# Kernel optimization log

Hardware: AMD Instinct MI355X
Metric: run time of the kernel (lower is better)

## Reference

```python
import jax, jax.numpy as jnp
import numpy as np

N_HEADS = 16
D_MODEL = 1024
D_K = D_MODEL // N_HEADS
NEG_INF = -1e9


def setup_inputs() -> dict:
    key = jax.random.key(0)
    ks = jax.random.split(key, 7)
    B, S, D = 4, 2048, D_MODEL
    scale = 1.0 / np.sqrt(D)
    return {
        "query": jax.random.normal(ks[0], (B, S, D), dtype=jnp.float32),
        "key": jax.random.normal(ks[1], (B, S, D), dtype=jnp.float32),
        "value": jax.random.normal(ks[2], (B, S, D), dtype=jnp.float32),
        "Wq": jax.random.normal(ks[3], (D, D), dtype=jnp.float32) * scale,
        "Wk": jax.random.normal(ks[4], (D, D), dtype=jnp.float32) * scale,
        "Wv": jax.random.normal(ks[5], (D, D), dtype=jnp.float32) * scale,
        "Wo": jax.random.normal(ks[6], (D, D), dtype=jnp.float32) * scale,
    }


def _split_heads(x):
    # (B, S, D) -> (B, H, S, d_k)
    B, S, _ = x.shape
    return x.reshape(B, S, N_HEADS, D_K).transpose(0, 2, 1, 3)


def reference(query, key, value, Wq, Wk, Wv, Wo):
    B, S, D = query.shape
    # nn.Linear(d, d, bias=False): y = x @ W.T ; here W is stored as [out, in]
    Q = _split_heads(query @ Wq.T)
    K = _split_heads(key @ Wk.T)
    V = _split_heads(value @ Wv.T)
    scores = jnp.einsum("bhqd,bhkd->bhqk", Q, K) / jnp.sqrt(jnp.float32(D_K))
    # causal mask: 0 on/below diagonal, -1e9 above
    causal = jnp.where(
        jnp.tril(jnp.ones((S, S), dtype=bool)), 0.0, NEG_INF
    ).astype(scores.dtype)
    scores = scores + causal[None, None, :, :]
    attn = jax.nn.softmax(scores, axis=-1)
    heads = jnp.einsum("bhqk,bhkd->bhqd", attn, V)
    concat = heads.transpose(0, 2, 1, 3).reshape(B, S, D)
    out = concat @ Wo.T
    return out  # dropout p=0.0 -> identity
```

## Files before the change

kernel.cpp:

```cpp
#include <hip/hip_runtime.h>
#include <hip/hip_bf16.h>

typedef short short8 __attribute__((ext_vector_type(8)));
typedef short short4v __attribute__((ext_vector_type(4)));
typedef float floatx4 __attribute__((ext_vector_type(4)));

constexpr int BATCH = 4;
constexpr int SEQ = 2048;
constexpr int DMODEL = 1024;
constexpr int NHEADS = 16;
constexpr int DKH = 64;
constexpr int MROWS = BATCH * SEQ;
constexpr size_t NE = (size_t)MROWS * DMODEL;
constexpr size_t WE = (size_t)DMODEL * DMODEL;
constexpr float SC = 0.18033688011112042f;

__device__ __forceinline__ short f2bf(float f) {
    unsigned u = __float_as_uint(f);
    u += 0x7fffu + ((u >> 16) & 1u);
    return (short)(u >> 16);
}

__device__ __forceinline__ short2 pk2(float a, float b) {
    __hip_bfloat162 h = __float22bfloat162_rn(float2{a, b});
    short2 r;
    __builtin_memcpy(&r, &h, 4);
    return r;
}

__device__ __forceinline__ void ld16(const void* g, void* l) {
    __builtin_amdgcn_global_load_lds(
        (const __attribute__((address_space(1))) unsigned int*)g,
        (__attribute__((address_space(3))) unsigned int*)l, 16, 0, 0);
}

__global__ __launch_bounds__(256) void f32_to_bf16(const float* __restrict__ s,
                                                   short* __restrict__ d, int n4) {
    int i = blockIdx.x * blockDim.x + threadIdx.x;
    const int stride = gridDim.x * blockDim.x;
    for (; i < n4; i += stride) {
        float4 f = ((const float4*)s)[i];
        short4v v;
        v[0] = f2bf(f.x); v[1] = f2bf(f.y); v[2] = f2bf(f.z); v[3] = f2bf(f.w);
        ((short4v*)d)[i] = v;
    }
}

__global__ __launch_bounds__(256) void cvt2(const float* __restrict__ s0,
                                            const float* __restrict__ s1,
                                            short* __restrict__ d0,
                                            short* __restrict__ d1, int n4) {
    const float* s = blockIdx.y ? s1 : s0;
    short* d = blockIdx.y ? d1 : d0;
    int i = blockIdx.x * blockDim.x + threadIdx.x;
    const int stride = gridDim.x * blockDim.x;
    for (; i < n4; i += stride) {
        float4 f = ((const float4*)s)[i];
        short4v v;
        v[0] = f2bf(f.x); v[1] = f2bf(f.y); v[2] = f2bf(f.z); v[3] = f2bf(f.w);
        ((short4v*)d)[i] = v;
    }
}

__global__ __launch_bounds__(256) void wcvt3(const float* __restrict__ a,
                                             const float* __restrict__ b,
                                             const float* __restrict__ c,
                                             short* __restrict__ dst, int n4) {
    const float* s = (blockIdx.y == 0) ? a : (blockIdx.y == 1) ? b : c;
    const float m = (blockIdx.y == 0) ? SC : 1.0f;
    short* d = dst + (size_t)blockIdx.y * (size_t)n4 * 4;
    int i = blockIdx.x * blockDim.x + threadIdx.x;
    const int stride = gridDim.x * blockDim.x;
    for (; i < n4; i += stride) {
        float4 f = ((const float4*)s)[i];
        short4v v;
        v[0] = f2bf(f.x * m); v[1] = f2bf(f.y * m);
        v[2] = f2bf(f.z * m); v[3] = f2bf(f.w * m);
        ((short4v*)d)[i] = v;
    }
}

template <int OUT_MODE>
__device__ __forceinline__ void gemm_body(const short* __restrict__ A,
                                          const short* __restrict__ B,
                                          void* __restrict__ Yp) {
    __shared__ __align__(16) short Asw[2][128 * 32];
    __shared__ __align__(16) short Bsw[2][128 * 32];

    const int tid = threadIdx.x;
    const int w = tid >> 6, l = tid & 63;
    const int lane16 = l & 15, quad = l >> 4;
    const int wm = (w >> 1) * 64, wn = (w & 1) * 64;
    const int m0 = blockIdx.x * 128, n0 = blockIdx.y * 128;
    const int fsw = (lane16 >> 1) & 3;

    auto stage = [&](int k0, int bufi) {
#pragma unroll
        for (int i = 0; i < 2; ++i) {
            const int id = i * 256 + tid;
            const int row = id >> 2, ch = id & 3;
            const int sch = ch ^ ((row >> 1) & 3);
            ld16(A + (size_t)(m0 + row) * DMODEL + k0 + sch * 8,
                 &Asw[bufi][(i * 256 + w * 64) * 8]);
            ld16(B + (size_t)(n0 + row) * DMODEL + k0 + sch * 8,
                 &Bsw[bufi][(i * 256 + w * 64) * 8]);
        }
    };

    floatx4 acc[4][4];
#pragma unroll
    for (int i = 0; i < 4; ++i)
#pragma unroll
        for (int j = 0; j < 4; ++j) acc[i][j] = {0.f, 0.f, 0.f, 0.f};

    constexpr int NT = DMODEL / 32;
    stage(0, 0);
    __syncthreads();

    for (int t = 0; t < NT; ++t) {
        const int cur = t & 1;
        if (t + 1 < NT) stage((t + 1) * 32, cur ^ 1);

        short8 af[4], bfr[4];
#pragma unroll
        for (int mi = 0; mi < 4; ++mi)
            af[mi] = *(const short8*)(&Asw[cur][(wm + mi * 16 + lane16) * 32 +
                                                ((quad ^ fsw) * 8)]);
#pragma unroll
        for (int ni = 0; ni < 4; ++ni)
            bfr[ni] = *(const short8*)(&Bsw[cur][(wn + ni * 16 + lane16) * 32 +
                                                 ((quad ^ fsw) * 8)]);
#pragma unroll
        for (int mi = 0; mi < 4; ++mi)
#pragma unroll
            for (int ni = 0; ni < 4; ++ni)
                acc[mi][ni] = __builtin_amdgcn_mfma_f32_16x16x32_bf16(af[mi], bfr[ni],
                                                                      acc[mi][ni], 0, 0, 0);
        __syncthreads();
    }

    const int gmb = m0 + wm, gnb = n0 + wn;
    if (OUT_MODE == 0) {
        short* Y = (short*)Yp;
#pragma unroll
        for (int mi = 0; mi < 4; ++mi)
#pragma unroll
            for (int ni = 0; ni < 4; ++ni) {
                const int gm = gmb + mi * 16 + quad * 4;
                const int gn = gnb + ni * 16 + lane16;
#pragma unroll
                for (int r = 0; r < 4; ++r)
                    Y[(size_t)(gm + r) * DMODEL + gn] = f2bf(acc[mi][ni][r]);
            }
    } else if (OUT_MODE == 1) {
        short* Y = (short*)Yp;
#pragma unroll
        for (int mi = 0; mi < 4; ++mi)
#pragma unroll
            for (int ni = 0; ni < 4; ++ni) {
                const int gm = gmb + mi * 16 + quad * 4;
                const int gn = gnb + ni * 16 + lane16;
                const int bb = gm >> 11, ss = gm & (SEQ - 1);
                const int hh = gn >> 6, dd = gn & 63;
                const size_t base = ((size_t)(bb * NHEADS + hh) * DKH + dd) * SEQ + ss;
                short4v vv;
#pragma unroll
                for (int r = 0; r < 4; ++r) vv[r] = f2bf(acc[mi][ni][r]);
                *(short4v*)(Y + base) = vv;
            }
    } else {
        float* Y = (float*)Yp;
#pragma unroll
        for (int mi = 0; mi < 4; ++mi)
#pragma unroll
            for (int ni = 0; ni < 4; ++ni) {
                const int gm = gmb + mi * 16 + quad * 4;
                const int gn = gnb + ni * 16 + lane16;
#pragma unroll
                for (int r = 0; r < 4; ++r)
                    Y[(size_t)(gm + r) * DMODEL + gn] = acc[mi][ni][r];
            }
    }
}

template <int OUT_MODE>
__global__ __launch_bounds__(256, 3) void gemm_nt(const short* __restrict__ A,
                                                  const short* __restrict__ B,
                                                  void* __restrict__ Yp) {
    gemm_body<OUT_MODE>(A, B, Yp);
}

__global__ __launch_bounds__(256, 3) void gemm_qk(const short* __restrict__ Aq,
                                                  const short* __restrict__ Ak,
                                                  const short* __restrict__ Wqk,
                                                  short* __restrict__ Yq,
                                                  short* __restrict__ Yk) {
    const int z = blockIdx.z;
    gemm_body<0>(z ? Ak : Aq, Wqk + (size_t)z * WE, z ? Yk : Yq);
}

__global__ __launch_bounds__(256, 4) void attn_fwd(const short* __restrict__ Qb,
                                                   const short* __restrict__ Kb,
                                                   const short* __restrict__ Vt,
                                                   short* __restrict__ Oc) {
    __shared__ __align__(16) short Kl[2][64 * 64];
    __shared__ __align__(16) short Vl[2][64 * 64];
    __shared__ __align__(16) short Plds[4][16][64];

    const int bh = blockIdx.x;
    const int qt = (int)(gridDim.y - 1) - blockIdx.y;
    const int b = bh >> 4, h = bh & 15;
    const int tid = threadIdx.x;
    const int w = tid >> 6, l = tid & 63;
    const int lane16 = l & 15, quad = l >> 4;

    const short* Qrow =
        Qb + ((size_t)b * SEQ + qt * 64 + w * 16 + lane16) * DMODEL + h * DKH;
    const short8 qf0 = *(const short8*)(Qrow + quad * 8);
    const short8 qf1 = *(const short8*)(Qrow + 32 + quad * 8);

    const int r0 = tid >> 3, c0 = tid & 7;
    const int sc0 = c0 ^ (r0 & 7);
    const short* Kg = Kb + (size_t)b * SEQ * DMODEL + h * DKH;
    const short* Vg = Vt + (size_t)bh * DKH * SEQ;

    short8 kra, krb, vra, vrb;
    kra = *(const short8*)(Kg + (size_t)r0 * DMODEL + c0 * 8);
    krb = *(const short8*)(Kg + (size_t)(r0 + 32) * DMODEL + c0 * 8);
    vra = *(const short8*)(Vg + (size_t)r0 * SEQ + c0 * 8);
    vrb = *(const short8*)(Vg + (size_t)(r0 + 32) * SEQ + c0 * 8);
    *(short8*)&Kl[0][r0 * 64 + sc0 * 8] = kra;
    *(short8*)&Kl[0][(r0 + 32) * 64 + sc0 * 8] = krb;
    *(short8*)&Vl[0][r0 * 64 + sc0 * 8] = vra;
    *(short8*)&Vl[0][(r0 + 32) * 64 + sc0 * 8] = vrb;
    if (qt > 0) {
        kra = *(const short8*)(Kg + (size_t)(64 + r0) * DMODEL + c0 * 8);
        krb = *(const short8*)(Kg + (size_t)(64 + r0 + 32) * DMODEL + c0 * 8);
        vra = *(const short8*)(Vg + (size_t)r0 * SEQ + 64 + c0 * 8);
        vrb = *(const short8*)(Vg + (size_t)(r0 + 32) * SEQ + 64 + c0 * 8);
    }

    floatx4 oacc[4];
#pragma unroll
    for (int ni = 0; ni < 4; ++ni) oacc[ni] = {0.f, 0.f, 0.f, 0.f};
    float Lp = 0.f;
    const int swz = lane16 & 7;
    const int psw = lane16 & 7;

    for (int kt = 0; kt <= qt; ++kt) {
        const int cur = kt & 1;
        __syncthreads();
        if (kt < qt) {
            const int nb = cur ^ 1;
            *(short8*)&Kl[nb][r0 * 64 + sc0 * 8] = kra;
            *(short8*)&Kl[nb][(r0 + 32) * 64 + sc0 * 8] = krb;
            *(short8*)&Vl[nb][r0 * 64 + sc0 * 8] = vra;
            *(short8*)&Vl[nb][(r0 + 32) * 64 + sc0 * 8] = vrb;
            if (kt + 1 < qt) {
                const int kn = (kt + 2) * 64;
                kra = *(const short8*)(Kg + (size_t)(kn + r0) * DMODEL + c0 * 8);
                krb = *(const short8*)(Kg + (size_t)(kn + r0 + 32) * DMODEL + c0 * 8);
                vra = *(const short8*)(Vg + (size_t)r0 * SEQ + kn + c0 * 8);
                vrb = *(const short8*)(Vg + (size_t)(r0 + 32) * SEQ + kn + c0 * 8);
            }
        }

        float p[4][4];
#pragma unroll
        for (int nt = 0; nt < 4; ++nt) {
            const short* kr = &Kl[cur][(nt * 16 + lane16) * 64];
            floatx4 st = {0.f, 0.f, 0.f, 0.f};
            st = __builtin_amdgcn_mfma_f32_16x16x32_bf16(
                *(const short8*)(kr + (quad ^ swz) * 8), qf0, st, 0, 0, 0);
            st = __builtin_amdgcn_mfma_f32_16x16x32_bf16(
                *(const short8*)(kr + ((4 + quad) ^ swz) * 8), qf1, st, 0, 0, 0);
#pragma unroll
            for (int r = 0; r < 4; ++r) p[nt][r] = st[r];
        }

#pragma unroll
        for (int nt = 0; nt < 4; ++nt)
#pragma unroll
            for (int r = 0; r < 4; ++r) p[nt][r] = __builtin_amdgcn_exp2f(p[nt][r]);

        if (kt == qt) {
            const int qloc = w * 16 + lane16;
#pragma unroll
            for (int nt = 0; nt < 4; ++nt)
#pragma unroll
                for (int r = 0; r < 4; ++r)
                    if (nt * 16 + quad * 4 + r > qloc) p[nt][r] = 0.f;
        }

        float rs01 = 0.f, rs23 = 0.f;
#pragma unroll
        for (int nt = 0; nt < 4; ++nt)
#pragma unroll
            for (int r = 0; r < 4; ++r) {
                if (nt < 2) rs01 += p[nt][r]; else rs23 += p[nt][r];
            }
        Lp += rs01 + rs23;

#pragma unroll
        for (int nt = 0; nt < 4; ++nt) {
            const short2 lo = pk2(p[nt][0], p[nt][1]);
            const short2 hi = pk2(p[nt][2], p[nt][3]);
            short4v pk;
            pk[0] = lo.x; pk[1] = lo.y; pk[2] = hi.x; pk[3] = hi.y;
            const int pch = (nt * 2 + (quad >> 1)) ^ psw;
            *(short4v*)&Plds[w][lane16][pch * 8 + (quad & 1) * 4] = pk;
        }
        const short8 pf0 = *(const short8*)&Plds[w][lane16][(quad ^ psw) * 8];
        const short8 pf1 = *(const short8*)&Plds[w][lane16][((4 + quad) ^ psw) * 8];

#pragma unroll
        for (int ni = 0; ni < 4; ++ni) {
            const short* vr = &Vl[cur][(ni * 16 + lane16) * 64];
            oacc[ni] = __builtin_amdgcn_mfma_f32_16x16x32_bf16(
                pf0, *(const short8*)(vr + (quad ^ swz) * 8), oacc[ni], 0, 0, 0);
            oacc[ni] = __builtin_amdgcn_mfma_f32_16x16x32_bf16(
                pf1, *(const short8*)(vr + ((4 + quad) ^ swz) * 8), oacc[ni], 0, 0, 0);
        }
    }

    float L = Lp + __shfl_xor(Lp, 16);
    L += __shfl_xor(L, 32);
    float linv[4];
#pragma unroll
    for (int r = 0; r < 4; ++r) linv[r] = 1.f / __shfl(L, quad * 4 + r);
#pragma unroll
    for (int r = 0; r < 4; ++r) {
        const int qg = qt * 64 + w * 16 + quad * 4 + r;
#pragma unroll
        for (int ni = 0; ni < 4; ++ni)
            Oc[((size_t)b * SEQ + qg) * DMODEL + h * DKH + ni * 16 + lane16] =
                f2bf(oacc[ni][r] * linv[r]);
    }
}

extern "C" void kernel_launch(void* const* d_in, const int* in_sizes, int n_in,
                              void* d_out, int out_size, void* d_ws, size_t ws_size,
                              hipStream_t stream) {
    const float* q = (const float*)d_in[0];
    const float* k = (const float*)d_in[1];
    const float* v = (const float*)d_in[2];
    const float* Wq = (const float*)d_in[3];
    const float* Wk = (const float*)d_in[4];
    const float* Wv = (const float*)d_in[5];
    const float* Wo = (const float*)d_in[6];

    short* Qb = (short*)d_ws;
    short* Kb = Qb + NE;
    short* Vt = Kb + NE;
    short* Cc = Vt + NE;
    short* Wqb = (short*)d_out;
    short* Wkb = Wqb + WE;
    short* Wvb = Wqb + 2 * WE;
    short* Kbf = Wqb + 3 * WE;
    short* Wob = Vt;

    dim3 gg(MROWS / 128, DMODEL / 128);
    dim3 gqk(MROWS / 128, DMODEL / 128, 2);
    dim3 ga(BATCH * NHEADS, SEQ / 64);
    const int actN4 = (int)(NE / 4), wN4 = (int)(WE / 4);

    wcvt3<<<dim3(256, 3), 256, 0, stream>>>(Wq, Wk, Wv, (short*)d_out, wN4);
    cvt2<<<dim3(1024, 2), 256, 0, stream>>>(q, k, Cc, Kbf, actN4);
    gemm_qk<<<gqk, 256, 0, stream>>>(Cc, Kbf, Wqb, Qb, Kb);
    f32_to_bf16<<<2048, 256, 0, stream>>>(v, Cc, actN4);
    gemm_nt<1><<<gg, 256, 0, stream>>>(Cc, Wvb, Vt);
    attn_fwd<<<ga, 256, 0, stream>>>(Qb, Kb, Vt, Cc);
    f32_to_bf16<<<512, 256, 0, stream>>>(Wo, Wob, wN4);
    gemm_nt<2><<<gg, 256, 0, stream>>>(Cc, Wob, d_out);
}
```

Measured before the change: 312.0 us.

## Use 256x256 GEMM tiles with 8 waves and interleaved split-K LDS pipeline

Enlarges the projection GEMM block tile from 128x128 to 256x256 and uses 512 threads (8 waves, each computing 128x64). Each 64-wide K step is split into two 32-wide sub-stages whose global-to-LDS loads are interleaved with the MFMA phases. Hand-written vmcnt waits plus barriers replace __syncthreads, and s_setprio raises priority around the MFMA bursts. The aim is more operand reuse per LDS byte and better overlap of loads with compute. The trade-off is that the V and output GEMMs now launch only 128 blocks on a 256-CU device, and register and LDS pressure per block rise.

Measured after the change: 328.5 us. +5.3%, slower.

```diff
diff --git a/kernel.cpp b/kernel.cpp
--- a/kernel.cpp
+++ b/kernel.cpp
@@ -32,6 +32,19 @@
     __builtin_amdgcn_global_load_lds(
         (const __attribute__((address_space(1))) unsigned int*)g,
         (__attribute__((address_space(3))) unsigned int*)l, 16, 0, 0);
+}
+
+__device__ __forceinline__ void sync_vm4() {
+    asm volatile("s_waitcnt vmcnt(4)" ::: "memory");
+    __builtin_amdgcn_sched_barrier(0);
+    __builtin_amdgcn_s_barrier();
+    __builtin_amdgcn_sched_barrier(0);
+}
+__device__ __forceinline__ void sync_vm0() {
+    asm volatile("s_waitcnt vmcnt(0)" ::: "memory");
+    __builtin_amdgcn_sched_barrier(0);
+    __builtin_amdgcn_s_barrier();
+    __builtin_amdgcn_sched_barrier(0);
 }
 
 __global__ __launch_bounds__(256) void f32_to_bf16(const float* __restrict__ s,
@@ -80,70 +93,99 @@
     }
 }
 
+template <int MH, int KS, bool RB>
+__device__ __forceinline__ void do_phase(const short* Ab, const short* Bb,
+                                         floatx4 (&acc)[8][4], short8 (&bfr)[4],
+                                         int wmw, int wnw, int lane16, int quad,
+                                         int fsw) {
+    if (RB) {
+#pragma unroll
+        for (int ni = 0; ni < 4; ++ni) {
+            const int row = wnw + ni * 16 + lane16;
+            bfr[ni] = *(const short8*)&Bb[KS * (256 * 32) + row * 32 +
+                                          ((quad ^ fsw) * 8)];
+        }
+    }
+    short8 af[4];
+#pragma unroll
+    for (int i = 0; i < 4; ++i) {
+        const int row = wmw + MH * 64 + i * 16 + lane16;
+        af[i] = *(const short8*)&Ab[KS * (256 * 32) + row * 32 +
+                                    ((quad ^ fsw) * 8)];
+    }
+    __builtin_amdgcn_s_setprio(1);
+#pragma unroll
+    for (int i = 0; i < 4; ++i)
+#pragma unroll
+        for (int ni = 0; ni < 4; ++ni)
+            acc[MH * 4 + i][ni] = __builtin_amdgcn_mfma_f32_16x16x32_bf16(
+                af[i], bfr[ni], acc[MH * 4 + i][ni], 0, 0, 0);
+    __builtin_amdgcn_s_setprio(0);
+}
+
 template <int OUT_MODE>
-__device__ __forceinline__ void gemm_body(const short* __restrict__ A,
-                                          const short* __restrict__ B,
-                                          void* __restrict__ Yp) {
-    __shared__ __align__(16) short Asw[2][128 * 32];
-    __shared__ __align__(16) short Bsw[2][128 * 32];
+__device__ __forceinline__ void gemm_body(const short* A, const short* B,
+                                          void* Yp) {
+    __shared__ __align__(16) short Asw[2][2][256 * 32];
+    __shared__ __align__(16) short Bsw[2][2][256 * 32];
 
     const int tid = threadIdx.x;
     const int w = tid >> 6, l = tid & 63;
     const int lane16 = l & 15, quad = l >> 4;
-    const int wm = (w >> 1) * 64, wn = (w & 1) * 64;
-    const int m0 = blockIdx.x * 128, n0 = blockIdx.y * 128;
+    const int wmw = (w >> 2) * 128, wnw = (w & 3) * 64;
+    const int m0 = blockIdx.x * 256, n0 = blockIdx.y * 256;
     const int fsw = (lane16 >> 1) & 3;
 
-    auto stage = [&](int k0, int bufi) {
-#pragma unroll
-        for (int i = 0; i < 2; ++i) {
-            const int id = i * 256 + tid;
-            const int row = id >> 2, ch = id & 3;
-            const int sch = ch ^ ((row >> 1) & 3);
-            ld16(A + (size_t)(m0 + row) * DMODEL + k0 + sch * 8,
-                 &Asw[bufi][(i * 256 + w * 64) * 8]);
-            ld16(B + (size_t)(n0 + row) * DMODEL + k0 + sch * 8,
-                 &Bsw[bufi][(i * 256 + w * 64) * 8]);
-        }
+    const int rr = tid >> 2;
+    const int cc = (tid & 3) ^ ((rr >> 1) & 3);
+    const int ldsA0 = (w * 64) * 8, ldsA1 = (512 + w * 64) * 8;
+
+    auto stA = [&](int k0, int bufi, int ks) {
+        const short* g = A + (size_t)m0 * DMODEL + k0 + ks * 32 + cc * 8;
+        ld16(g + (size_t)rr * DMODEL, &Asw[bufi][ks][ldsA0]);
+        ld16(g + (size_t)(rr + 128) * DMODEL, &Asw[bufi][ks][ldsA1]);
     };
-
-    floatx4 acc[4][4];
-#pragma unroll
-    for (int i = 0; i < 4; ++i)
+    auto stB = [&](int k0, int bufi, int ks) {
+        const short* g = B + (size_t)n0 * DMODEL + k0 + ks * 32 + cc * 8;
+        ld16(g + (size_t)rr * DMODEL, &Bsw[bufi][ks][ldsA0]);
+        ld16(g + (size_t)(rr + 128) * DMODEL, &Bsw[bufi][ks][ldsA1]);
+    };
+
+    floatx4 acc[8][4];
+#pragma unroll
+    for (int i = 0; i < 8; ++i)
 #pragma unroll
         for (int j = 0; j < 4; ++j) acc[i][j] = {0.f, 0.f, 0.f, 0.f};
 
-    constexpr int NT = DMODEL / 32;
-    stage(0, 0);
-    __syncthreads();
-
+    constexpr int NT = DMODEL / 64;
+    stA(0, 0, 0); stB(0, 0, 0); stA(0, 0, 1); stB(0, 0, 1);
+    sync_vm4();
+
+    short8 bfr[4];
     for (int t = 0; t < NT; ++t) {
-        const int cur = t & 1;
-        if (t + 1 < NT) stage((t + 1) * 32, cur ^ 1);
-
-        short8 af[4], bfr[4];
-#pragma unroll
-        for (int mi = 0; mi < 4; ++mi)
-            af[mi] = *(const short8*)(&Asw[cur][(wm + mi * 16 + lane16) * 32 +
-                                                ((quad ^ fsw) * 8)]);
-#pragma unroll
-        for (int ni = 0; ni < 4; ++ni)
-            bfr[ni] = *(const short8*)(&Bsw[cur][(wn + ni * 16 + lane16) * 32 +
-                                                 ((quad ^ fsw) * 8)]);
-#pragma unroll
-        for (int mi = 0; mi < 4; ++mi)
-#pragma unroll
-            for (int ni = 0; ni < 4; ++ni)
-                acc[mi][ni] = __builtin_amdgcn_mfma_f32_16x16x32_bf16(af[mi], bfr[ni],
-                                                                      acc[mi][ni], 0, 0, 0);
-        __syncthreads();
-    }
-
-    const int gmb = m0 + wm, gnb = n0 + wn;
+        const int cur = t & 1, nxt = cur ^ 1;
+        const short* Ab = &Asw[cur][0][0];
+        const short* Bb = &Bsw[cur][0][0];
+        const int k1 = (t + 1) * 64;
+        const bool more = (t + 1 < NT);
+
+        if (more) stA(k1, nxt, 0);
+        do_phase<0, 0, true>(Ab, Bb, acc, bfr, wmw, wnw, lane16, quad, fsw);
+        if (more) stB(k1, nxt, 0);
+        do_phase<1, 0, false>(Ab, Bb, acc, bfr, wmw, wnw, lane16, quad, fsw);
+        if (more) sync_vm4(); else sync_vm0();
+        if (more) stA(k1, nxt, 1);
+        do_phase<0, 1, true>(Ab, Bb, acc, bfr, wmw, wnw, lane16, quad, fsw);
+        if (more) stB(k1, nxt, 1);
+        do_phase<1, 1, false>(Ab, Bb, acc, bfr, wmw, wnw, lane16, quad, fsw);
+        if (more) sync_vm4();
+    }
+
+    const int gmb = m0 + wmw, gnb = n0 + wnw;
     if (OUT_MODE == 0) {
         short* Y = (short*)Yp;
 #pragma unroll
-        for (int mi = 0; mi < 4; ++mi)
+        for (int mi = 0; mi < 8; ++mi)
 #pragma unroll
             for (int ni = 0; ni < 4; ++ni) {
                 const int gm = gmb + mi * 16 + quad * 4;
@@ -155,7 +197,7 @@
     } else if (OUT_MODE == 1) {
         short* Y = (short*)Yp;
 #pragma unroll
-        for (int mi = 0; mi < 4; ++mi)
+        for (int mi = 0; mi < 8; ++mi)
 #pragma unroll
             for (int ni = 0; ni < 4; ++ni) {
                 const int gm = gmb + mi * 16 + quad * 4;
@@ -171,7 +213,7 @@
     } else {
         float* Y = (float*)Yp;
 #pragma unroll
-        for (int mi = 0; mi < 4; ++mi)
+        for (int mi = 0; mi < 8; ++mi)
 #pragma unroll
             for (int ni = 0; ni < 4; ++ni) {
                 const int gm = gmb + mi * 16 + quad * 4;
@@ -184,13 +226,13 @@
 }
 
 template <int OUT_MODE>
-__global__ __launch_bounds__(256, 3) void gemm_nt(const short* __restrict__ A,
+__global__ __launch_bounds__(512, 2) void gemm_nt(const short* __restrict__ A,
                                                   const short* __restrict__ B,
                                                   void* __restrict__ Yp) {
     gemm_body<OUT_MODE>(A, B, Yp);
 }
 
-__global__ __launch_bounds__(256, 3) void gemm_qk(const short* __restrict__ Aq,
+__global__ __launch_bounds__(512, 2) void gemm_qk(const short* __restrict__ Aq,
                                                   const short* __restrict__ Ak,
                                                   const short* __restrict__ Wqk,
                                                   short* __restrict__ Yq,
@@ -359,17 +401,17 @@
     short* Kbf = Wqb + 3 * WE;
     short* Wob = Vt;
 
-    dim3 gg(MROWS / 128, DMODEL / 128);
-    dim3 gqk(MROWS / 128, DMODEL / 128, 2);
+    dim3 gg(MROWS / 256, DMODEL / 256);
+    dim3 gqk(MROWS / 256, DMODEL / 256, 2);
     dim3 ga(BATCH * NHEADS, SEQ / 64);
     const int actN4 = (int)(NE / 4), wN4 = (int)(WE / 4);
 
     wcvt3<<<dim3(256, 3), 256, 0, stream>>>(Wq, Wk, Wv, (short*)d_out, wN4);
     cvt2<<<dim3(1024, 2), 256, 0, stream>>>(q, k, Cc, Kbf, actN4);
-    gemm_qk<<<gqk, 256, 0, stream>>>(Cc, Kbf, Wqb, Qb, Kb);
+    gemm_qk<<<gqk, 512, 0, stream>>>(Cc, Kbf, Wqb, Qb, Kb);
     f32_to_bf16<<<2048, 256, 0, stream>>>(v, Cc, actN4);
-    gemm_nt<1><<<gg, 256, 0, stream>>>(Cc, Wvb, Vt);
+    gemm_nt<1><<<gg, 512, 0, stream>>>(Cc, Wvb, Vt);
     attn_fwd<<<ga, 256, 0, stream>>>(Qb, Kb, Vt, Cc);
     f32_to_bf16<<<512, 256, 0, stream>>>(Wo, Wob, wN4);
-    gemm_nt<2><<<gg, 256, 0, stream>>>(Cc, Wob, d_out);
-}
+    gemm_nt<2><<<gg, 512, 0, stream>>>(Cc, Wob, d_out);
+}
```
